# Kernel tuning notes

Hardware: AMD Instinct MI355X
Metric: run time of the kernel (lower is better)

The kernel has to match this reference:

```python
import jax, jax.numpy as jnp
import numpy as np

EMBED_DIM = 1024
NUM_HEADS = 16
HEAD_DIM = EMBED_DIM // NUM_HEADS


def setup_inputs() -> dict:
    key = jax.random.key(0)
    k1, k2, k3, k4, k5 = jax.random.split(key, 5)
    B, S, D = 1, 4096, EMBED_DIM
    scale = 0.02
    return {
        "input": jax.random.normal(k1, (B, S, D), dtype=jnp.float32),
        "Wqkv": jax.random.normal(k2, (D, 3 * D), dtype=jnp.float32) * scale,
        "bqkv": jax.random.normal(k3, (3 * D,), dtype=jnp.float32) * scale,
        "Wo": jax.random.normal(k4, (D, D), dtype=jnp.float32) * scale,
        "bo": jax.random.normal(k5, (D,), dtype=jnp.float32) * scale,
    }


def reference(input, Wqkv, bqkv, Wo, bo):
    B, S, D = input.shape
    H, Hd = NUM_HEADS, HEAD_DIM
    qkv = input @ Wqkv + bqkv                        # [B, S, 3D]
    qkv = qkv.reshape(B, S, 3, H, Hd)
    qkv = jnp.transpose(qkv, (2, 0, 3, 1, 4))        # [3, B, H, S, Hd]
    q, k, v = qkv[0], qkv[1], qkv[2]
    scores = jnp.einsum("bhsd,bhtd->bhst", q, k) / (Hd ** 0.5)  # [B,H,S,S]
    causal = jnp.tril(jnp.ones((S, S), dtype=bool))[None, None]
    scores = jnp.where(causal, scores, -jnp.inf)
    attn = jax.nn.softmax(scores, axis=-1)
    out = jnp.einsum("bhst,bhtd->bhsd", attn, v)     # [B,H,S,Hd]
    out = jnp.transpose(out, (0, 2, 1, 3)).reshape(B, S, D)
    return out @ Wo + bo
```

## Files before the change

### kernel.cpp

```cpp
#include <hip/hip_runtime.h>

typedef __bf16 bf16;
typedef __bf16 bf16x8 __attribute__((ext_vector_type(8)));
typedef float f32x4 __attribute__((ext_vector_type(4)));
typedef float f32x16 __attribute__((ext_vector_type(16)));
typedef unsigned u32x2 __attribute__((ext_vector_type(2)));

#define MFMA16(a, b, c) __builtin_amdgcn_mfma_f32_16x16x32_bf16((a), (b), (c), 0, 0, 0)
#define MFMA32(a, b, c) __builtin_amdgcn_mfma_f32_32x32x16_bf16((a), (b), (c), 0, 0, 0)

typedef const __attribute__((address_space(1))) uint32_t glb_u32;
typedef __attribute__((address_space(3))) uint32_t lds_u32;
#define GLOAD16(gp, lp) __builtin_amdgcn_global_load_lds((glb_u32*)(gp), (lds_u32*)(lp), 16, 0, 0)

__global__ __launch_bounds__(256) void k_convX(const float* __restrict__ in, bf16* __restrict__ out) {
    size_t i = ((size_t)blockIdx.x * 256 + threadIdx.x) * 8;
    float4 a = *(const float4*)(in + i);
    float4 b = *(const float4*)(in + i + 4);
    bf16 e[8];
    e[0] = (bf16)a.x; e[1] = (bf16)a.y; e[2] = (bf16)a.z; e[3] = (bf16)a.w;
    e[4] = (bf16)b.x; e[5] = (bf16)b.y; e[6] = (bf16)b.z; e[7] = (bf16)b.w;
    uint4 u; __builtin_memcpy(&u, e, 16);
    *(uint4*)(out + i) = u;
}

__global__ __launch_bounds__(256) void k_tconv(const float* __restrict__ in, bf16* __restrict__ out,
                                               int R, int C) {
    __shared__ float tile[64][65];
    int bx = blockIdx.x, by = blockIdx.y;
    int t = threadIdx.x;
    for (int i = 0; i < 16; ++i) {
        int e = i * 256 + t; int r = e >> 6, c = e & 63;
        tile[r][c] = in[(size_t)(by * 64 + r) * C + bx * 64 + c];
    }
    __syncthreads();
    for (int i = 0; i < 16; ++i) {
        int e = i * 256 + t; int r = e >> 6, c = e & 63;
        out[(size_t)(bx * 64 + r) * R + by * 64 + c] = (bf16)tile[c][r];
    }
}

__global__ __launch_bounds__(256) void k_kpack(const uint4* __restrict__ in, uint4* __restrict__ out) {
    int c = blockIdx.x * 256 + threadIdx.x;
    int h = c >> 15;
    int r = c & 32767;
    int tile = r >> 8, kst = (r >> 6) & 3, l = r & 63;
    int t = tile * 32 + (l & 31);
    int dc = kst * 2 + (l >> 5);
    out[c] = in[((size_t)h * 4096 + t) * 8 + dc];
}

__global__ __launch_bounds__(256) void k_vtrans(const bf16* __restrict__ V, uint4* __restrict__ Vfr) {
    __shared__ bf16 tl[64][68];
    int t0 = blockIdx.x * 64;
    int h = blockIdx.y;
    int t = threadIdx.x;
    const bf16* Vh = V + (size_t)h * 4096 * 64;
    #pragma unroll
    for (int i = 0; i < 2; ++i) {
        int c = i * 256 + t; int row = c >> 3, ch = c & 7;
        uint4 v = *(const uint4*)(Vh + (size_t)(t0 + row) * 64 + ch * 8);
        bf16 e[8]; __builtin_memcpy(e, &v, 16);
        #pragma unroll
        for (int j = 0; j < 8; ++j) tl[row][ch * 8 + j] = e[j];
    }
    __syncthreads();
    uint4* Vfh = Vfr + (size_t)h * 32768;
    #pragma unroll
    for (int i = 0; i < 2; ++i) {
        int c = i * 256 + t; int d = c >> 3, tch = c & 7;
        bf16 e[8];
        #pragma unroll
        for (int j = 0; j < 8; ++j) e[j] = tl[tch * 8 + j][d];
        uint4 u; __builtin_memcpy(&u, e, 16);
        int tile = blockIdx.x * 2 + (tch >> 2);
        int chunk = tile * 256 + ((d >> 5) * 2 + ((tch >> 1) & 1)) * 64 + (d & 31) + 32 * (tch & 1);
        Vfh[chunk] = u;
    }
}

__device__ __forceinline__ void gemm128_core(const bf16* __restrict__ A, const bf16* __restrict__ Bt,
                                             int r0, int c0, int Kd, char* As, char* Bs,
                                             f32x4 (&acc)[4][4]) {
    int t = threadIdx.x, l = t & 63, w = t >> 6;
    int g = l >> 4, li = l & 15;
    int wr = w >> 1, wc = w & 1;
    for (int k0 = 0; k0 < Kd; k0 += 64) {
        __syncthreads();
        #pragma unroll
        for (int i = 0; i < 4; ++i) {
            int slot = i * 256 + t;
            int row = slot >> 3;
            int ch  = (slot & 7) ^ (row & 7);
            int base = (i * 256 + w * 64) * 16;
            GLOAD16(A  + (size_t)(r0 + row) * Kd + k0 + ch * 8, As + base);
            GLOAD16(Bt + (size_t)(c0 + row) * Kd + k0 + ch * 8, Bs + base);
        }
        __syncthreads();
        __builtin_amdgcn_s_setprio(1);
        #pragma unroll
        for (int kk = 0; kk < 2; ++kk) {
            bf16x8 af[4], bfr[4];
            #pragma unroll
            for (int m = 0; m < 4; ++m) {
                int row = wr * 64 + m * 16 + li;
                af[m] = *(const bf16x8*)(As + ((row * 128 + kk * 64 + g * 16) ^ ((row & 7) << 4)));
            }
            #pragma unroll
            for (int n = 0; n < 4; ++n) {
                int row = wc * 64 + n * 16 + li;
                bfr[n] = *(const bf16x8*)(Bs + ((row * 128 + kk * 64 + g * 16) ^ ((row & 7) << 4)));
            }
            #pragma unroll
            for (int m = 0; m < 4; ++m)
                #pragma unroll
                for (int n = 0; n < 4; ++n)
                    acc[m][n] = MFMA16(af[m], bfr[n], acc[m][n]);
        }
        __builtin_amdgcn_s_setprio(0);
    }
}

__global__ __launch_bounds__(256) void k_gemm_qkv(const bf16* __restrict__ Xb, const bf16* __restrict__ WqkvT,
                                                  const float* __restrict__ bqkv,
                                                  bf16* __restrict__ Q, bf16* __restrict__ K,
                                                  bf16* __restrict__ V) {
    __shared__ __align__(16) char As[16384];
    __shared__ __align__(16) char Bs[16384];
    int r0 = blockIdx.y * 128, c0 = blockIdx.x * 128;
    f32x4 acc[4][4] = {};
    gemm128_core(Xb, WqkvT, r0, c0, 1024, As, Bs, acc);
    int t = threadIdx.x, l = t & 63, w = t >> 6;
    int g = l >> 4, li = l & 15;
    int wr = w >> 1, wc = w & 1;
    int colbase = c0 + wc * 64;
    int sec = colbase >> 10;
    int head = (colbase & 1023) >> 6;
    bf16* dst = (sec == 0) ? Q : (sec == 1) ? K : V;
    float scale = (sec == 0) ? 0.125f * 1.44269504f : 1.0f;
    #pragma unroll
    for (int m = 0; m < 4; ++m)
        #pragma unroll
        for (int n = 0; n < 4; ++n) {
            int hd = n * 16 + li;
            float bias = bqkv[colbase + hd];
            #pragma unroll
            for (int r = 0; r < 4; ++r) {
                int row = r0 + wr * 64 + m * 16 + g * 4 + r;
                dst[(size_t)(head * 4096 + row) * 64 + hd] = (bf16)((acc[m][n][r] + bias) * scale);
            }
        }
}

__global__ __launch_bounds__(256) void k_gemm_out(const bf16* __restrict__ Ob, const bf16* __restrict__ WoT,
                                                  const float* __restrict__ bo, float* __restrict__ out) {
    __shared__ __align__(16) char As[16384];
    __shared__ __align__(16) char Bs[16384];
    int r0 = blockIdx.y * 128, c0 = blockIdx.x * 128;
    f32x4 acc[4][4] = {};
    gemm128_core(Ob, WoT, r0, c0, 1024, As, Bs, acc);
    int t = threadIdx.x, l = t & 63, w = t >> 6;
    int g = l >> 4, li = l & 15;
    int wr = w >> 1, wc = w & 1;
    #pragma unroll
    for (int m = 0; m < 4; ++m)
        #pragma unroll
        for (int n = 0; n < 4; ++n) {
            int col = c0 + wc * 64 + n * 16 + li;
            float bias = bo[col];
            #pragma unroll
            for (int r = 0; r < 4; ++r) {
                int row = r0 + wr * 64 + m * 16 + g * 4 + r;
                out[(size_t)row * 1024 + col] = acc[m][n][r] + bias;
            }
        }
}

__device__ __forceinline__ unsigned pkbf(float a, float b) {
    bf16 h0 = (bf16)a, h1 = (bf16)b;
    unsigned short u0, u1;
    __builtin_memcpy(&u0, &h0, 2); __builtin_memcpy(&u1, &h1, 2);
    return (unsigned)u0 | ((unsigned)u1 << 16);
}

__global__ __launch_bounds__(128) void k_attn(const bf16* __restrict__ Q, const uint4* __restrict__ Kfr,
                                              const uint4* __restrict__ Vfr, bf16* __restrict__ O) {
    __shared__ float Op[32][64];
    __shared__ float Ml[2][32];
    int bid = blockIdx.x;
    int h = bid & 15;
    int u = bid >> 4;
    int jj = (u < 64) ? u : 191 - u;
    int w = threadIdx.x >> 6;
    int l = threadIdx.x & 63;
    int lc = l & 31, hi = l >> 5;
    int hi4 = hi * 4, hi8 = hi * 8;
    const bf16* Qh = Q + (size_t)h * 4096 * 64;
    const uint4* Kh = Kfr + (size_t)h * 32768;
    const uint4* Vh = Vfr + (size_t)h * 32768;
    int nt = jj + 1;
    int hA = (nt + 1) >> 1;
    int tb = w ? hA : 0;
    int te = w ? nt : hA;

    f32x16 oacc[2] = {};
    float m = -1e30f, lsum = 0.f;
    uint4 kA[4], vA[4], kB[4], vB[4];
    bf16x8 qf[4];
    #pragma unroll
    for (int kst = 0; kst < 4; ++kst)
        qf[kst] = *(const bf16x8*)(Qh + (size_t)(jj * 32 + lc) * 64 + kst * 16 + hi8);

    auto compute = [&](int tt, uint4 (&kf)[4], uint4 (&vf)[4]) {
        f32x16 sacc = {};
        __builtin_amdgcn_s_setprio(1);
        #pragma unroll
        for (int kst = 0; kst < 4; ++kst) {
            bf16x8 kk; __builtin_memcpy(&kk, &kf[kst], 16);
            sacc = MFMA32(kk, qf[kst], sacc);
        }
        __builtin_amdgcn_s_setprio(0);
        if (tt == jj) {
            #pragma unroll
            for (int r = 0; r < 16; ++r) {
                int tloc = (r & 3) + 8 * (r >> 2) + hi4;
                if (tloc > lc) sacc[r] = -1e30f;
            }
        }
        float t8[8];
        #pragma unroll
        for (int r = 0; r < 8; ++r) t8[r] = fmaxf(sacc[r], sacc[r + 8]);
        float ta = fmaxf(fmaxf(t8[0], t8[1]), t8[2]);
        float tb3 = fmaxf(fmaxf(t8[3], t8[4]), t8[5]);
        float tc = fmaxf(t8[6], t8[7]);
        float pm = fmaxf(fmaxf(ta, tb3), tc);
        pm = fmaxf(pm, __shfl_xor(pm, 32));
        if (!__all(pm - m <= 8.0f)) {
            float mn = fmaxf(m, pm);
            float al = exp2f(m - mn);
            #pragma unroll
            for (int r = 0; r < 16; ++r) {
                int ql = (r & 3) + 8 * (r >> 2) + hi4;
                float alb = __shfl(al, ql);
                oacc[0][r] *= alb;
                oacc[1][r] *= alb;
            }
            lsum *= al;
            m = mn;
        }
        float pv[16];
        float rs0 = 0.f, rs1 = 0.f;
        #pragma unroll
        for (int r = 0; r < 8; ++r) {
            pv[r]     = exp2f(sacc[r] - m);     rs0 += pv[r];
            pv[r + 8] = exp2f(sacc[r + 8] - m); rs1 += pv[r + 8];
        }
        lsum += rs0 + rs1;
        #pragma unroll
        for (int ks = 0; ks < 2; ++ks) {
            int b = ks * 8;
            unsigned a0 = pkbf(pv[b + 0], pv[b + 1]), a1 = pkbf(pv[b + 2], pv[b + 3]);
            unsigned b0 = pkbf(pv[b + 4], pv[b + 5]), b1 = pkbf(pv[b + 6], pv[b + 7]);
            u32x2 r0 = __builtin_amdgcn_permlane32_swap(a0, b0, false, false);
            u32x2 r1 = __builtin_amdgcn_permlane32_swap(a1, b1, false, false);
            unsigned wsq[4] = { r0[0], r1[0], r0[1], r1[1] };
            bf16x8 pa; __builtin_memcpy(&pa, wsq, 16);
            __builtin_amdgcn_s_setprio(1);
            #pragma unroll
            for (int jt = 0; jt < 2; ++jt) {
                bf16x8 vv; __builtin_memcpy(&vv, &vf[jt * 2 + ks], 16);
                oacc[jt] = MFMA32(pa, vv, oacc[jt]);
            }
            __builtin_amdgcn_s_setprio(0);
        }
    };

    if (te > tb) {
        #pragma unroll
        for (int i = 0; i < 4; ++i) {
            kA[i] = Kh[(size_t)tb * 256 + i * 64 + l];
            vA[i] = Vh[(size_t)tb * 256 + i * 64 + l];
        }
        int i = tb;
        for (; i + 2 <= te; i += 2) {
            const uint4* Kn = Kh + (size_t)(i + 1) * 256;
            const uint4* Vn = Vh + (size_t)(i + 1) * 256;
            #pragma unroll
            for (int q = 0; q < 4; ++q) { kB[q] = Kn[q * 64 + l]; vB[q] = Vn[q * 64 + l]; }
            compute(i, kA, vA);
            if (i + 2 < te) {
                const uint4* K2 = Kh + (size_t)(i + 2) * 256;
                const uint4* V2 = Vh + (size_t)(i + 2) * 256;
                #pragma unroll
                for (int q = 0; q < 4; ++q) { kA[q] = K2[q * 64 + l]; vA[q] = V2[q * 64 + l]; }
            }
            compute(i + 1, kB, vB);
        }
        if ((te - tb) & 1) compute(te - 1, kA, vA);
    }
    lsum += __shfl_xor(lsum, 32);

    if (w == 1) {
        #pragma unroll
        for (int r = 0; r < 16; ++r) {
            int ql = (r & 3) + 8 * (r >> 2) + hi4;
            Op[ql][lc]      = oacc[0][r];
            Op[ql][32 + lc] = oacc[1][r];
        }
        if (hi == 0) { Ml[0][lc] = m; Ml[1][lc] = lsum; }
    }
    __syncthreads();
    if (w == 0) {
        float mo = Ml[0][lc], lo = Ml[1][lc];
        float mm = fmaxf(m, mo);
        float alr = exp2f(m - mm), alo = exp2f(mo - mm);
        float lf = lsum * alr + lo * alo;
        float inv = 1.0f / lf;
        float fr = alr * inv, fo = alo * inv;
        int q0 = jj * 32;
        #pragma unroll
        for (int r = 0; r < 16; ++r) {
            int ql = (r & 3) + 8 * (r >> 2) + hi4;
            float frb = __shfl(fr, ql), fob = __shfl(fo, ql);
            float o0 = oacc[0][r] * frb + Op[ql][lc]      * fob;
            float o1 = oacc[1][r] * frb + Op[ql][32 + lc] * fob;
            int row = q0 + ql;
            O[(size_t)row * 1024 + h * 64 + lc]      = (bf16)o0;
            O[(size_t)row * 1024 + h * 64 + 32 + lc] = (bf16)o1;
        }
    }
}

extern "C" void kernel_launch(void* const* d_in, const int* in_sizes, int n_in,
                              void* d_out, int out_size, void* d_ws, size_t ws_size,
                              hipStream_t stream) {
    const float* X    = (const float*)d_in[0];
    const float* Wqkv = (const float*)d_in[1];
    const float* bqkv = (const float*)d_in[2];
    const float* Wo   = (const float*)d_in[3];
    const float* bo   = (const float*)d_in[4];
    float* out = (float*)d_out;

    char* ws = (char*)d_ws;
    const size_t MB = 1024 * 1024;
    bf16*  Xb    = (bf16*)(ws);
    bf16*  WqkvT = (bf16*)(ws + 8  * MB);
    bf16*  WoT   = (bf16*)(ws + 14 * MB);
    bf16*  Qb    = (bf16*)(ws + 16 * MB);
    bf16*  Kb    = (bf16*)(ws + 24 * MB);
    bf16*  Vb    = (bf16*)(ws + 32 * MB);
    uint4* Kfr   = (uint4*)(ws + 40 * MB);
    uint4* Vfr   = (uint4*)(ws + 48 * MB);
    bf16*  Ob    = Xb;

    k_convX<<<2048, 256, 0, stream>>>(X, Xb);
    k_tconv<<<dim3(48, 16), 256, 0, stream>>>(Wqkv, WqkvT, 1024, 3072);
    k_tconv<<<dim3(16, 16), 256, 0, stream>>>(Wo, WoT, 1024, 1024);
    k_gemm_qkv<<<dim3(24, 32), 256, 0, stream>>>(Xb, WqkvT, bqkv, Qb, Kb, Vb);
    k_kpack<<<2048, 256, 0, stream>>>((const uint4*)Kb, Kfr);
    k_vtrans<<<dim3(64, 16), 256, 0, stream>>>(Vb, Vfr);
    k_attn<<<2048, 128, 0, stream>>>(Qb, Kfr, Vfr, Ob);
    k_gemm_out<<<dim3(8, 32), 256, 0, stream>>>(Ob, WoT, bo, out);
}
```

Baseline: 161.5 us.

## Fuse K/V fragment packing into QKV GEMM epilogue and retile output GEMM

The QKV GEMM epilogue now writes K and V straight into the fragment-packed layouts the attention kernel reads. This removes the separate kpack and vtrans kernels, along with their extra global round trips and launches. The output projection GEMM moves to 128x64 tiles, giving 512 blocks instead of 256 so more CUs are busy. In exchange, the K epilogue does scattered 2-byte stores, and the smaller output tiles reuse each loaded tile less.

```diff
diff --git a/kernel.cpp b/kernel.cpp
--- a/kernel.cpp
+++ b/kernel.cpp
@@ -40,45 +40,6 @@
     }
 }
 
-__global__ __launch_bounds__(256) void k_kpack(const uint4* __restrict__ in, uint4* __restrict__ out) {
-    int c = blockIdx.x * 256 + threadIdx.x;
-    int h = c >> 15;
-    int r = c & 32767;
-    int tile = r >> 8, kst = (r >> 6) & 3, l = r & 63;
-    int t = tile * 32 + (l & 31);
-    int dc = kst * 2 + (l >> 5);
-    out[c] = in[((size_t)h * 4096 + t) * 8 + dc];
-}
-
-__global__ __launch_bounds__(256) void k_vtrans(const bf16* __restrict__ V, uint4* __restrict__ Vfr) {
-    __shared__ bf16 tl[64][68];
-    int t0 = blockIdx.x * 64;
-    int h = blockIdx.y;
-    int t = threadIdx.x;
-    const bf16* Vh = V + (size_t)h * 4096 * 64;
-    #pragma unroll
-    for (int i = 0; i < 2; ++i) {
-        int c = i * 256 + t; int row = c >> 3, ch = c & 7;
-        uint4 v = *(const uint4*)(Vh + (size_t)(t0 + row) * 64 + ch * 8);
-        bf16 e[8]; __builtin_memcpy(e, &v, 16);
-        #pragma unroll
-        for (int j = 0; j < 8; ++j) tl[row][ch * 8 + j] = e[j];
-    }
-    __syncthreads();
-    uint4* Vfh = Vfr + (size_t)h * 32768;
-    #pragma unroll
-    for (int i = 0; i < 2; ++i) {
-        int c = i * 256 + t; int d = c >> 3, tch = c & 7;
-        bf16 e[8];
-        #pragma unroll
-        for (int j = 0; j < 8; ++j) e[j] = tl[tch * 8 + j][d];
-        uint4 u; __builtin_memcpy(&u, e, 16);
-        int tile = blockIdx.x * 2 + (tch >> 2);
-        int chunk = tile * 256 + ((d >> 5) * 2 + ((tch >> 1) & 1)) * 64 + (d & 31) + 32 * (tch & 1);
-        Vfh[chunk] = u;
-    }
-}
-
 __device__ __forceinline__ void gemm128_core(const bf16* __restrict__ A, const bf16* __restrict__ Bt,
                                              int r0, int c0, int Kd, char* As, char* Bs,
                                              f32x4 (&acc)[4][4]) {
@@ -123,8 +84,8 @@
 
 __global__ __launch_bounds__(256) void k_gemm_qkv(const bf16* __restrict__ Xb, const bf16* __restrict__ WqkvT,
                                                   const float* __restrict__ bqkv,
-                                                  bf16* __restrict__ Q, bf16* __restrict__ K,
-                                                  bf16* __restrict__ V) {
+                                                  bf16* __restrict__ Q, bf16* __restrict__ Kfr,
+                                                  bf16* __restrict__ Vfr) {
     __shared__ __align__(16) char As[16384];
     __shared__ __align__(16) char Bs[16384];
     int r0 = blockIdx.y * 128, c0 = blockIdx.x * 128;
@@ -136,41 +97,116 @@
     int colbase = c0 + wc * 64;
     int sec = colbase >> 10;
     int head = (colbase & 1023) >> 6;
-    bf16* dst = (sec == 0) ? Q : (sec == 1) ? K : V;
-    float scale = (sec == 0) ? 0.125f * 1.44269504f : 1.0f;
-    #pragma unroll
-    for (int m = 0; m < 4; ++m)
-        #pragma unroll
-        for (int n = 0; n < 4; ++n) {
-            int hd = n * 16 + li;
-            float bias = bqkv[colbase + hd];
-            #pragma unroll
-            for (int r = 0; r < 4; ++r) {
-                int row = r0 + wr * 64 + m * 16 + g * 4 + r;
-                dst[(size_t)(head * 4096 + row) * 64 + hd] = (bf16)((acc[m][n][r] + bias) * scale);
-            }
-        }
+    if (sec == 0) {
+        const float scale = 0.125f * 1.44269504f;
+        #pragma unroll
+        for (int m = 0; m < 4; ++m)
+            #pragma unroll
+            for (int n = 0; n < 4; ++n) {
+                int hd = n * 16 + li;
+                float bias = bqkv[colbase + hd];
+                #pragma unroll
+                for (int r = 0; r < 4; ++r) {
+                    int row = r0 + wr * 64 + m * 16 + g * 4 + r;
+                    Q[(size_t)(head * 4096 + row) * 64 + hd] = (bf16)((acc[m][n][r] + bias) * scale);
+                }
+            }
+    } else if (sec == 1) {
+        bf16* dstK = Kfr + (size_t)head * 262144;
+        #pragma unroll
+        for (int m = 0; m < 4; ++m) {
+            int tbase = r0 + wr * 64 + m * 16 + g * 4;
+            size_t tpart = (size_t)(tbase >> 5) * 2048 + (size_t)(tbase & 31) * 8;
+            #pragma unroll
+            for (int n = 0; n < 4; ++n) {
+                int hd = n * 16 + li;
+                float bias = bqkv[colbase + hd];
+                size_t A0 = tpart + (size_t)(hd >> 4) * 512 + (size_t)((hd >> 3) & 1) * 256 + (hd & 7);
+                #pragma unroll
+                for (int r = 0; r < 4; ++r)
+                    dstK[A0 + (size_t)r * 8] = (bf16)(acc[m][n][r] + bias);
+            }
+        }
+    } else {
+        bf16* dstV = Vfr + (size_t)head * 262144;
+        #pragma unroll
+        for (int m = 0; m < 4; ++m) {
+            int tbase = r0 + wr * 64 + m * 16 + g * 4;
+            size_t tpart = (size_t)(tbase >> 5) * 2048 + (size_t)((tbase >> 4) & 1) * 512
+                         + (size_t)((tbase >> 3) & 1) * 256 + (tbase & 7);
+            #pragma unroll
+            for (int n = 0; n < 4; ++n) {
+                int hd = n * 16 + li;
+                float bias = bqkv[colbase + hd];
+                size_t A0 = tpart + (size_t)(hd >> 5) * 1024 + (size_t)(hd & 31) * 8;
+                bf16 e4[4];
+                #pragma unroll
+                for (int r = 0; r < 4; ++r) e4[r] = (bf16)(acc[m][n][r] + bias);
+                unsigned long long pk; __builtin_memcpy(&pk, e4, 8);
+                *(unsigned long long*)(dstV + A0) = pk;
+            }
+        }
+    }
 }
 
 __global__ __launch_bounds__(256) void k_gemm_out(const bf16* __restrict__ Ob, const bf16* __restrict__ WoT,
                                                   const float* __restrict__ bo, float* __restrict__ out) {
     __shared__ __align__(16) char As[16384];
-    __shared__ __align__(16) char Bs[16384];
-    int r0 = blockIdx.y * 128, c0 = blockIdx.x * 128;
-    f32x4 acc[4][4] = {};
-    gemm128_core(Ob, WoT, r0, c0, 1024, As, Bs, acc);
+    __shared__ __align__(16) char Bs[8192];
+    int r0 = blockIdx.y * 128, c0 = blockIdx.x * 64;
     int t = threadIdx.x, l = t & 63, w = t >> 6;
     int g = l >> 4, li = l & 15;
-    int wr = w >> 1, wc = w & 1;
+    f32x4 acc[2][4] = {};
+    for (int k0 = 0; k0 < 1024; k0 += 64) {
+        __syncthreads();
+        #pragma unroll
+        for (int i = 0; i < 4; ++i) {
+            int slot = i * 256 + t;
+            int row = slot >> 3;
+            int ch  = (slot & 7) ^ (row & 7);
+            int base = (i * 256 + w * 64) * 16;
+            GLOAD16(Ob + (size_t)(r0 + row) * 1024 + k0 + ch * 8, As + base);
+        }
+        #pragma unroll
+        for (int i = 0; i < 2; ++i) {
+            int slot = i * 256 + t;
+            int row = slot >> 3;
+            int ch  = (slot & 7) ^ (row & 7);
+            int base = (i * 256 + w * 64) * 16;
+            GLOAD16(WoT + (size_t)(c0 + row) * 1024 + k0 + ch * 8, Bs + base);
+        }
+        __syncthreads();
+        __builtin_amdgcn_s_setprio(1);
+        #pragma unroll
+        for (int kk = 0; kk < 2; ++kk) {
+            bf16x8 af[2], bfr[4];
+            #pragma unroll
+            for (int m = 0; m < 2; ++m) {
+                int row = w * 32 + m * 16 + li;
+                af[m] = *(const bf16x8*)(As + ((row * 128 + kk * 64 + g * 16) ^ ((row & 7) << 4)));
+            }
+            #pragma unroll
+            for (int n = 0; n < 4; ++n) {
+                int row = n * 16 + li;
+                bfr[n] = *(const bf16x8*)(Bs + ((row * 128 + kk * 64 + g * 16) ^ ((row & 7) << 4)));
+            }
+            #pragma unroll
+            for (int m = 0; m < 2; ++m)
+                #pragma unroll
+                for (int n = 0; n < 4; ++n)
+                    acc[m][n] = MFMA16(af[m], bfr[n], acc[m][n]);
+        }
+        __builtin_amdgcn_s_setprio(0);
+    }
     #pragma unroll
-    for (int m = 0; m < 4; ++m)
+    for (int m = 0; m < 2; ++m)
         #pragma unroll
         for (int n = 0; n < 4; ++n) {
-            int col = c0 + wc * 64 + n * 16 + li;
+            int col = c0 + n * 16 + li;
             float bias = bo[col];
             #pragma unroll
             for (int r = 0; r < 4; ++r) {
-                int row = r0 + wr * 64 + m * 16 + g * 4 + r;
+                int row = r0 + w * 32 + m * 16 + g * 4 + r;
                 out[(size_t)row * 1024 + col] = acc[m][n][r] + bias;
             }
         }
@@ -347,8 +383,6 @@
     bf16*  WqkvT = (bf16*)(ws + 8  * MB);
     bf16*  WoT   = (bf16*)(ws + 14 * MB);
     bf16*  Qb    = (bf16*)(ws + 16 * MB);
-    bf16*  Kb    = (bf16*)(ws + 24 * MB);
-    bf16*  Vb    = (bf16*)(ws + 32 * MB);
     uint4* Kfr   = (uint4*)(ws + 40 * MB);
     uint4* Vfr   = (uint4*)(ws + 48 * MB);
     bf16*  Ob    = Xb;
@@ -356,9 +390,7 @@
     k_convX<<<2048, 256, 0, stream>>>(X, Xb);
     k_tconv<<<dim3(48, 16), 256, 0, stream>>>(Wqkv, WqkvT, 1024, 3072);
     k_tconv<<<dim3(16, 16), 256, 0, stream>>>(Wo, WoT, 1024, 1024);
-    k_gemm_qkv<<<dim3(24, 32), 256, 0, stream>>>(Xb, WqkvT, bqkv, Qb, Kb, Vb);
-    k_kpack<<<2048, 256, 0, stream>>>((const uint4*)Kb, Kfr);
-    k_vtrans<<<dim3(64, 16), 256, 0, stream>>>(Vb, Vfr);
+    k_gemm_qkv<<<dim3(24, 32), 256, 0, stream>>>(Xb, WqkvT, bqkv, Qb, (bf16*)Kfr, (bf16*)Vfr);
     k_attn<<<2048, 128, 0, stream>>>(Qb, Kfr, Vfr, Ob);
-    k_gemm_out<<<dim3(8, 32), 256, 0, stream>>>(Ob, WoT, bo, out);
-}
+    k_gemm_out<<<dim3(16, 32), 256, 0, stream>>>(Ob, WoT, bo, out);
+}
```

Result: faster. 151.3 us (-6.3%).
